# Kernel tuning notes

Measured on AMD Instinct MI355X. Metric: run time of the kernel, lower is better.

The kernel has to match this reference:

```python
import jax, jax.numpy as jnp
import numpy as np

B, N, D = 32, 2048, 512
Q, C = 8, 1024
COMMIT_W = 0.02


def setup_inputs() -> dict:
    key = jax.random.key(0)
    kx, kc = jax.random.split(key)
    x = jax.random.normal(kx, (B, N, D), dtype=jnp.float32)
    codebooks = jax.random.normal(kc, (Q, C, D), dtype=jnp.float32)  # per-quantizer embed tables
    return {"x": x, "codebooks": codebooks}


def _quantize(residual, embed):
    # residual: (B,N,D), embed: (C,D)
    flat = residual.reshape(-1, residual.shape[-1])  # (B*N, D)
    dist = (
        jnp.sum(flat * flat, axis=-1, keepdims=True)
        - 2.0 * (flat @ embed.T)
        + jnp.sum(embed * embed, axis=-1)
    )  # (B*N, C)
    idx = jnp.argmin(dist, axis=-1)  # (B*N,)
    q = embed[idx].reshape(residual.shape)  # codebook gather
    # commitment loss: mse(residual, stopgrad(quantized))
    commit = jnp.mean((jax.lax.stop_gradient(q) - residual) ** 2)
    # straight-through estimator
    q_st = residual + jax.lax.stop_gradient(q - residual)
    return idx.reshape(residual.shape[:-1]), q_st, commit


def reference(x, codebooks):
    residual = x
    quantized_out = jnp.zeros_like(x)
    all_indices = []
    all_losses = []
    for qi in range(Q):
        idx, quantized, commit = _quantize(residual, codebooks[qi])
        residual = residual - jax.lax.stop_gradient(quantized)
        quantized_out = quantized_out + quantized
        all_indices.append(idx)
        all_losses.append(commit * COMMIT_W)
    all_indices = jnp.stack(all_indices, axis=-1)  # (B, N, Q) int
    all_losses = jnp.stack(all_losses, axis=-1)  # (Q,)
    final_commit_loss = jnp.sum(all_losses)
    return quantized_out, all_indices, all_losses, final_commit_loss
```

## Files before the change

### kernel.cpp

```cpp
#include <hip/hip_runtime.h>

#define TOKENS   65536
#define DDIM     512
#define NQ       8
#define NCODES   1024
#define COMMIT_W 0.02

#define MT       32
#define NBLOCKS  (TOKENS / MT)
#define KSPLIT   384

#define OFF_IDX  ((size_t)TOKENS * DDIM)
#define OFF_LOSS (OFF_IDX + (size_t)TOKENS * NQ)
#define OFF_TOT  (OFF_LOSS + NQ)

typedef _Float16 f16;
typedef _Float16 f16x8 __attribute__((ext_vector_type(8)));
typedef float    f32x4 __attribute__((ext_vector_type(4)));

__device__ __forceinline__ bool better(float d, int i, float bd, int bi) {
  return (d < bd) || (d == bd && i < bi);
}

__device__ __forceinline__ void ins4(float dd, int c, float cd[4], int ci[4]) {
  if (better(dd, c, cd[3], ci[3])) {
    if (better(dd, c, cd[1], ci[1])) {
      if (better(dd, c, cd[0], ci[0])) {
        cd[3]=cd[2]; ci[3]=ci[2]; cd[2]=cd[1]; ci[2]=ci[1];
        cd[1]=cd[0]; ci[1]=ci[0]; cd[0]=dd; ci[0]=c;
      } else {
        cd[3]=cd[2]; ci[3]=ci[2]; cd[2]=cd[1]; ci[2]=ci[1];
        cd[1]=dd; ci[1]=c;
      }
    } else {
      if (better(dd, c, cd[2], ci[2])) { cd[3]=cd[2]; ci[3]=ci[2]; cd[2]=dd; ci[2]=c; }
      else { cd[3]=dd; ci[3]=c; }
    }
  }
}

__device__ __forceinline__ void merge4(float cd[4], int ci[4], const int m) {
  const float b0 = __shfl_xor(cd[0], m, 64), b1 = __shfl_xor(cd[1], m, 64),
              b2 = __shfl_xor(cd[2], m, 64), b3 = __shfl_xor(cd[3], m, 64);
  const int   o0 = __shfl_xor(ci[0], m, 64), o1 = __shfl_xor(ci[1], m, 64),
              o2 = __shfl_xor(ci[2], m, 64), o3 = __shfl_xor(ci[3], m, 64);
  float L0, L1, L2, L3; int M0, M1, M2, M3;
  if (better(b3, o3, cd[0], ci[0])) { L0 = b3; M0 = o3; } else { L0 = cd[0]; M0 = ci[0]; }
  if (better(b2, o2, cd[1], ci[1])) { L1 = b2; M1 = o2; } else { L1 = cd[1]; M1 = ci[1]; }
  if (better(b1, o1, cd[2], ci[2])) { L2 = b1; M2 = o1; } else { L2 = cd[2]; M2 = ci[2]; }
  if (better(b0, o0, cd[3], ci[3])) { L3 = b0; M3 = o0; } else { L3 = cd[3]; M3 = ci[3]; }
  if (better(L2, M2, L0, M0)) { float t=L0; L0=L2; L2=t; int u=M0; M0=M2; M2=u; }
  if (better(L3, M3, L1, M1)) { float t=L1; L1=L3; L3=t; int u=M1; M1=M3; M3=u; }
  if (better(L1, M1, L0, M0)) { float t=L0; L0=L1; L1=t; int u=M0; M0=M1; M1=u; }
  if (better(L3, M3, L2, M2)) { float t=L2; L2=L3; L3=t; int u=M2; M2=M3; M3=u; }
  cd[0]=L0; ci[0]=M0; cd[1]=L1; ci[1]=M1; cd[2]=L2; ci[2]=M2; cd[3]=L3; ci[3]=M3;
}

__device__ __forceinline__ float pw128_row_sq(const float* __restrict__ a) {
  float r0 = __fmul_rn(a[0], a[0]), r1 = __fmul_rn(a[1], a[1]);
  float r2 = __fmul_rn(a[2], a[2]), r3 = __fmul_rn(a[3], a[3]);
  float r4 = __fmul_rn(a[4], a[4]), r5 = __fmul_rn(a[5], a[5]);
  float r6 = __fmul_rn(a[6], a[6]), r7 = __fmul_rn(a[7], a[7]);
  for (int i = 8; i < 128; i += 8) {
    r0 = __fadd_rn(r0, __fmul_rn(a[i + 0], a[i + 0]));
    r1 = __fadd_rn(r1, __fmul_rn(a[i + 1], a[i + 1]));
    r2 = __fadd_rn(r2, __fmul_rn(a[i + 2], a[i + 2]));
    r3 = __fadd_rn(r3, __fmul_rn(a[i + 3], a[i + 3]));
    r4 = __fadd_rn(r4, __fmul_rn(a[i + 4], a[i + 4]));
    r5 = __fadd_rn(r5, __fmul_rn(a[i + 5], a[i + 5]));
    r6 = __fadd_rn(r6, __fmul_rn(a[i + 6], a[i + 6]));
    r7 = __fadd_rn(r7, __fmul_rn(a[i + 7], a[i + 7]));
  }
  return __fadd_rn(__fadd_rn(__fadd_rn(r0, r1), __fadd_rn(r2, r3)),
                   __fadd_rn(__fadd_rn(r4, r5), __fadd_rn(r6, r7)));
}

__global__ void prep_kernel(const float* __restrict__ cb, float* __restrict__ eef,
                            double* __restrict__ lossAcc) {
  const int code = blockIdx.x * blockDim.x + threadIdx.x;
  if (code == 0) {
#pragma unroll
    for (int j = 0; j < NQ; ++j) lossAcc[j] = 0.0;
  }
  if (code < NQ * NCODES) {
    const float* e = cb + (size_t)code * DDIM;
    const float p0 = pw128_row_sq(e), p1 = pw128_row_sq(e + 128);
    const float p2 = pw128_row_sq(e + 256), p3 = pw128_row_sq(e + 384);
    eef[code] = __fadd_rn(__fadd_rn(p0, p1), __fadd_rn(p2, p3));
  }
}

__global__ void cvt_kernel(const float* __restrict__ cb, f16* __restrict__ cbH) {
  const size_t base = ((size_t)blockIdx.x * 256 + threadIdx.x) * 8;
  const float4 v0 = *(const float4*)(cb + base);
  const float4 v1 = *(const float4*)(cb + base + 4);
  f16x8 h;
  h[0] = (f16)v0.x; h[1] = (f16)v0.y; h[2] = (f16)v0.z; h[3] = (f16)v0.w;
  h[4] = (f16)v1.x; h[5] = (f16)v1.y; h[6] = (f16)v1.z; h[7] = (f16)v1.w;
  *(f16x8*)(cbH + base) = h;
}

__global__ void __launch_bounds__(256, 2)
rvq_main(const float* __restrict__ x, const float* __restrict__ cb,
         const f16* __restrict__ cbH, const float* __restrict__ eef,
         double* __restrict__ lossAcc, float* __restrict__ outq,
         float* __restrict__ outidx) {
  __shared__ float  r_t[DDIM * MT];
  __shared__ __align__(16) char smem_u[MT * 128 * 2];
  __shared__ float  ee_lds[NCODES];
  __shared__ int    hist[MT][NQ];
  __shared__ double wred[4];

  f16*   ra  = (f16*)smem_u;
  float* wcd = (float*)smem_u;
  int*   wci = (int*)(smem_u + 2048);

  const int tid  = threadIdx.x;
  const int lane = tid & 63;
  const int wv   = tid >> 6;
  const int cbase = wv << 8;
  const int tokR = tid >> 3;
  const int part = tid & 7;
  const int blockTok = blockIdx.x * MT;

  {
    const int tm = tid & 31, kp = tid >> 5;
    const float* xr = x + (size_t)(blockTok + tm) * DDIM;
#pragma unroll
    for (int i = 0; i < 16; ++i) {
      const int d4 = (kp + i * 8) << 2;
      const float4 v = *(const float4*)(xr + d4);
      r_t[(d4 + 0) * MT + tm] = v.x;
      r_t[(d4 + 1) * MT + tm] = v.y;
      r_t[(d4 + 2) * MT + tm] = v.z;
      r_t[(d4 + 3) * MT + tm] = v.w;
    }
  }
  __syncthreads();

  const int la15 = lane & 15;
  const int kg8  = (lane >> 4) << 3;
  const int swz  = (la15 & 7) << 3;

  for (int qi = 0; qi < NQ; ++qi) {
    const float* cbq   = cb  + (size_t)qi * NCODES * DDIM;
    const f16*   cbq16 = cbH + (size_t)qi * NCODES * DDIM;
    const float* enq   = eef + qi * NCODES;

#pragma unroll
    for (int j = 0; j < 4; ++j) ee_lds[tid + j * 256] = enq[tid + j * 256];

    f32x4 acc[16][2];
#pragma unroll
    for (int mt = 0; mt < 16; ++mt) {
      acc[mt][0] = (f32x4){0.f, 0.f, 0.f, 0.f};
      acc[mt][1] = (f32x4){0.f, 0.f, 0.f, 0.f};
    }

    for (int ch = 0; ch < 4; ++ch) {
      __syncthreads();
      {
        const int tok  = tid & 31;
        const int ko   = tid >> 5;
        const int tswz = (tok & 7) << 3;
#pragma unroll
        for (int i = 0; i < 2; ++i) {
          const int kl = (ko + (i << 3)) << 3;
          const int kg = (ch << 7) + kl;
          f16x8 h;
#pragma unroll
          for (int j = 0; j < 8; ++j) h[j] = (f16)r_t[(kg + j) * MT + tok];
          *(f16x8*)&ra[tok * 128 + (kl ^ tswz)] = h;
        }
      }
      __syncthreads();
#pragma unroll
      for (int s = 0; s < 4; ++s) {
        const int kk = (s << 5) + kg8;
        const f16x8 b0 = *(const f16x8*)&ra[la15 * 128 + (kk ^ swz)];
        const f16x8 b1 = *(const f16x8*)&ra[(la15 + 16) * 128 + (kk ^ swz)];
        const f16* ap = cbq16 + (size_t)(cbase + la15) * DDIM + (ch << 7) + kk;
#pragma unroll
        for (int mt = 0; mt < 16; ++mt) {
          const f16x8 a = *(const f16x8*)(ap + (size_t)(mt << 4) * DDIM);
          acc[mt][0] = __builtin_amdgcn_mfma_f32_16x16x32_f16(a, b0, acc[mt][0], 0, 0, 0);
          acc[mt][1] = __builtin_amdgcn_mfma_f32_16x16x32_f16(a, b1, acc[mt][1], 0, 0, 0);
        }
      }
    }
    __syncthreads();

    float cd0[4], cd1[4]; int ci0[4], ci1[4];
#pragma unroll
    for (int s = 0; s < 4; ++s) {
      cd0[s] = 3.0e38f; ci0[s] = 0x7fffffff;
      cd1[s] = 3.0e38f; ci1[s] = 0x7fffffff;
    }
    const int rbase = cbase + ((lane >> 4) << 2);
#pragma unroll
    for (int mt = 0; mt < 16; ++mt) {
#pragma unroll
      for (int r = 0; r < 4; ++r) {
        const int code = rbase + (mt << 4) + r;
        const float eb = ee_lds[code];
        ins4(fmaf(-2.0f, acc[mt][0][r], eb), code, cd0, ci0);
        ins4(fmaf(-2.0f, acc[mt][1][r], eb), code, cd1, ci1);
      }
    }
    merge4(cd0, ci0, 16); merge4(cd0, ci0, 32);
    merge4(cd1, ci1, 16); merge4(cd1, ci1, 32);

    if (lane < 16) {
      const int w32 = wv << 5;
#pragma unroll
      for (int s = 0; s < 4; ++s) {
        wcd[(w32 + lane) * 4 + s]      = cd0[s];
        wci[(w32 + lane) * 4 + s]      = ci0[s];
        wcd[(w32 + lane + 16) * 4 + s] = cd1[s];
        wci[(w32 + lane + 16) * 4 + s] = ci1[s];
      }
    }
    __syncthreads();

    if (tid < 128) {
      const int tok4 = tid >> 2, cnd = tid & 3;
      float fd[4]; int fi[4];
#pragma unroll
      for (int s = 0; s < 4; ++s) { fd[s] = 3.0e38f; fi[s] = 0x7fffffff; }
      for (int w2 = 0; w2 < 4; ++w2) {
#pragma unroll
        for (int s = 0; s < 4; ++s) {
          const int e = ((w2 << 5) + tok4) * 4 + s;
          ins4(wcd[e], wci[e], fd, fi);
        }
      }
      const int cme = fi[cnd];

      float blk;
      {
        const int kb = cnd * 128;
        float a[8];
#pragma unroll
        for (int j = 0; j < 8; ++j) {
          const float v = r_t[(kb + j) * MT + tok4];
          a[j] = __fmul_rn(v, v);
        }
        for (int i = 8; i < 128; i += 8) {
#pragma unroll
          for (int j = 0; j < 8; ++j) {
            const float v = r_t[(kb + i + j) * MT + tok4];
            a[j] = __fadd_rn(a[j], __fmul_rn(v, v));
          }
        }
        blk = __fadd_rn(__fadd_rn(__fadd_rn(a[0], a[1]), __fadd_rn(a[2], a[3])),
                        __fadd_rn(__fadd_rn(a[4], a[5]), __fadd_rn(a[6], a[7])));
      }
      const float pw256 = __fadd_rn(blk, __shfl_xor(blk, 1, 64));
      const float rr    = __fadd_rn(pw256, __shfl_xor(pw256, 2, 64));

      const float* ep = cbq + (size_t)cme * DDIM;
      float Sa = 0.f, Sb = 0.f;
      for (int kb = 0; kb < DDIM; kb += 8) {
        const float4 e0 = *(const float4*)(ep + kb);
        const float4 e1 = *(const float4*)(ep + kb + 4);
        const float ev[8] = {e0.x, e0.y, e0.z, e0.w, e1.x, e1.y, e1.z, e1.w};
        float rv[8];
#pragma unroll
        for (int j = 0; j < 8; ++j) rv[j] = r_t[(kb + j) * MT + tok4];
        if (kb < KSPLIT) {
#pragma unroll
          for (int j = 0; j < 8; ++j) Sa = __fmaf_rn(rv[j], ev[j], Sa);
        } else {
#pragma unroll
          for (int j = 0; j < 8; ++j) Sb = __fmaf_rn(rv[j], ev[j], Sb);
        }
      }
      const float cross = __fadd_rn(Sa, Sb);
      const float u = __fsub_rn(rr, __fmul_rn(2.0f, cross));
      float dW = __fadd_rn(u, enq[cme]);
      int   cW = cme;
#pragma unroll
      for (int m = 1; m <= 2; m <<= 1) {
        const float od = __shfl_xor(dW, m, 64);
        const int   oc = __shfl_xor(cW, m, 64);
        if (better(od, oc, dW, cW)) { dW = od; cW = oc; }
      }
      if (cnd == 0) {
        hist[tok4][qi] = cW;
        outidx[(size_t)(blockTok + tok4) * NQ + qi] = (float)cW;
      }
    }
    __syncthreads();

    const int wc = hist[tokR][qi];
    const float* ew = cbq + (size_t)wc * DDIM;
    double lssq = 0.0;
    for (int i = 0; i < 16; ++i) {
      const int d4 = (part + i * 8) << 2;
      const float4 qv = *(const float4*)(ew + d4);
      const float qa[4] = {qv.x, qv.y, qv.z, qv.w};
#pragma unroll
      for (int e = 0; e < 4; ++e) {
        const float r  = r_t[(d4 + e) * MT + tokR];
        const float a  = __fsub_rn(qa[e], r);
        const float qs = __fadd_rn(r, a);
        const float rn = __fsub_rn(r, qs);
        r_t[(d4 + e) * MT + tokR] = rn;
        lssq += (double)a * (double)a;
      }
    }
#pragma unroll
    for (int off = 32; off; off >>= 1) lssq += __shfl_down(lssq, off, 64);
    if ((tid & 63) == 0) wred[tid >> 6] = lssq;
    __syncthreads();
    if (tid == 0) atomicAdd(&lossAcc[qi], wred[0] + wred[1] + wred[2] + wred[3]);
  }

  {
    for (int i = 0; i < 16; ++i) {
      const int d4 = (part + i * 8) << 2;
      const float4 xv = *(const float4*)(x + (size_t)(blockTok + tokR) * DDIM + d4);
      float r[4]  = {xv.x, xv.y, xv.z, xv.w};
      float qa[4] = {0.f, 0.f, 0.f, 0.f};
#pragma unroll
      for (int j = 0; j < NQ; ++j) {
        const int hj = hist[tokR][j];
        const float4 ev = *(const float4*)(cb + ((size_t)j * NCODES + hj) * DDIM + d4);
        const float qv[4] = {ev.x, ev.y, ev.z, ev.w};
#pragma unroll
        for (int e = 0; e < 4; ++e) {
          const float a  = __fsub_rn(qv[e], r[e]);
          const float qs = __fadd_rn(r[e], a);
          r[e]  = __fsub_rn(r[e], qs);
          qa[e] = __fadd_rn(qa[e], qs);
        }
      }
      float4 pk; pk.x = qa[0]; pk.y = qa[1]; pk.z = qa[2]; pk.w = qa[3];
      *(float4*)(outq + (size_t)(blockTok + tokR) * DDIM + d4) = pk;
    }
  }
}

__global__ void loss_fin(const double* __restrict__ lossAcc,
                         float* __restrict__ outLoss,
                         float* __restrict__ outTot) {
  if (threadIdx.x == 0 && blockIdx.x == 0) {
    double tot = 0.0;
    for (int qi = 0; qi < NQ; ++qi) {
      const double v = lossAcc[qi] * (COMMIT_W / ((double)TOKENS * (double)DDIM));
      outLoss[qi] = (float)v;
      tot += v;
    }
    *outTot = (float)tot;
  }
}

extern "C" void kernel_launch(void* const* d_in, const int* in_sizes, int n_in,
                              void* d_out, int out_size, void* d_ws, size_t ws_size,
                              hipStream_t stream) {
  const float* x  = (const float*)d_in[0];
  const float* cb = (const float*)d_in[1];
  float* out = (float*)d_out;

  double* lossAcc = (double*)d_ws;
  float*  eef     = (float*)((char*)d_ws + 256);
  f16*    cbH     = (f16*)((char*)d_ws + 65536);

  prep_kernel<<<dim3(32), dim3(256), 0, stream>>>(cb, eef, lossAcc);
  cvt_kernel<<<dim3(2048), dim3(256), 0, stream>>>(cb, cbH);
  rvq_main<<<dim3(NBLOCKS), dim3(256), 0, stream>>>(x, cb, cbH, eef, lossAcc,
                                                    out, out + OFF_IDX);
  loss_fin<<<dim3(1), dim3(64), 0, stream>>>(lossAcc, out + OFF_LOSS, out + OFF_TOT);
}
```

Before: 4.038 ms.

## Double block to 512 threads, halving per-wave codebook slice

```diff
diff --git a/kernel.cpp b/kernel.cpp
--- a/kernel.cpp
+++ b/kernel.cpp
@@ -7,6 +7,7 @@
 #define COMMIT_W 0.02
 
 #define MT       32
+#define NT       512
 #define NBLOCKS  (TOKENS / MT)
 #define KSPLIT   384
 
@@ -100,35 +101,33 @@
   *(f16x8*)(cbH + base) = h;
 }
 
-__global__ void __launch_bounds__(256, 2)
+__global__ void __launch_bounds__(NT, 4)
 rvq_main(const float* __restrict__ x, const float* __restrict__ cb,
          const f16* __restrict__ cbH, const float* __restrict__ eef,
          double* __restrict__ lossAcc, float* __restrict__ outq,
          float* __restrict__ outidx) {
   __shared__ float  r_t[DDIM * MT];
-  __shared__ __align__(16) char smem_u[MT * 128 * 2];
+  __shared__ __align__(16) char smem_u[8192];
   __shared__ float  ee_lds[NCODES];
   __shared__ int    hist[MT][NQ];
-  __shared__ double wred[4];
+  __shared__ double wred[8];
 
   f16*   ra  = (f16*)smem_u;
   float* wcd = (float*)smem_u;
-  int*   wci = (int*)(smem_u + 2048);
+  int*   wci = (int*)(smem_u + 4096);
 
   const int tid  = threadIdx.x;
   const int lane = tid & 63;
   const int wv   = tid >> 6;
-  const int cbase = wv << 8;
-  const int tokR = tid >> 3;
-  const int part = tid & 7;
+  const int cbase = wv << 7;
   const int blockTok = blockIdx.x * MT;
 
   {
     const int tm = tid & 31, kp = tid >> 5;
     const float* xr = x + (size_t)(blockTok + tm) * DDIM;
 #pragma unroll
-    for (int i = 0; i < 16; ++i) {
-      const int d4 = (kp + i * 8) << 2;
+    for (int i = 0; i < 8; ++i) {
+      const int d4 = (kp + i * 16) << 2;
       const float4 v = *(const float4*)(xr + d4);
       r_t[(d4 + 0) * MT + tm] = v.x;
       r_t[(d4 + 1) * MT + tm] = v.y;
@@ -148,11 +147,11 @@
     const float* enq   = eef + qi * NCODES;
 
 #pragma unroll
-    for (int j = 0; j < 4; ++j) ee_lds[tid + j * 256] = enq[tid + j * 256];
-
-    f32x4 acc[16][2];
-#pragma unroll
-    for (int mt = 0; mt < 16; ++mt) {
+    for (int j = 0; j < 2; ++j) ee_lds[tid + j * NT] = enq[tid + j * NT];
+
+    f32x4 acc[8][2];
+#pragma unroll
+    for (int mt = 0; mt < 8; ++mt) {
       acc[mt][0] = (f32x4){0.f, 0.f, 0.f, 0.f};
       acc[mt][1] = (f32x4){0.f, 0.f, 0.f, 0.f};
     }
@@ -163,15 +162,12 @@
         const int tok  = tid & 31;
         const int ko   = tid >> 5;
         const int tswz = (tok & 7) << 3;
-#pragma unroll
-        for (int i = 0; i < 2; ++i) {
-          const int kl = (ko + (i << 3)) << 3;
-          const int kg = (ch << 7) + kl;
-          f16x8 h;
-#pragma unroll
-          for (int j = 0; j < 8; ++j) h[j] = (f16)r_t[(kg + j) * MT + tok];
-          *(f16x8*)&ra[tok * 128 + (kl ^ tswz)] = h;
-        }
+        const int kl   = ko << 3;
+        const int kg   = (ch << 7) + kl;
+        f16x8 h;
+#pragma unroll
+        for (int j = 0; j < 8; ++j) h[j] = (f16)r_t[(kg + j) * MT + tok];
+        *(f16x8*)&ra[tok * 128 + (kl ^ tswz)] = h;
       }
       __syncthreads();
 #pragma unroll
@@ -181,7 +177,7 @@
         const f16x8 b1 = *(const f16x8*)&ra[(la15 + 16) * 128 + (kk ^ swz)];
         const f16* ap = cbq16 + (size_t)(cbase + la15) * DDIM + (ch << 7) + kk;
 #pragma unroll
-        for (int mt = 0; mt < 16; ++mt) {
+        for (int mt = 0; mt < 8; ++mt) {
           const f16x8 a = *(const f16x8*)(ap + (size_t)(mt << 4) * DDIM);
           acc[mt][0] = __builtin_amdgcn_mfma_f32_16x16x32_f16(a, b0, acc[mt][0], 0, 0, 0);
           acc[mt][1] = __builtin_amdgcn_mfma_f32_16x16x32_f16(a, b1, acc[mt][1], 0, 0, 0);
@@ -198,7 +194,7 @@
     }
     const int rbase = cbase + ((lane >> 4) << 2);
 #pragma unroll
-    for (int mt = 0; mt < 16; ++mt) {
+    for (int mt = 0; mt < 8; ++mt) {
 #pragma unroll
       for (int r = 0; r < 4; ++r) {
         const int code = rbase + (mt << 4) + r;
@@ -227,7 +223,7 @@
       float fd[4]; int fi[4];
 #pragma unroll
       for (int s = 0; s < 4; ++s) { fd[s] = 3.0e38f; fi[s] = 0x7fffffff; }
-      for (int w2 = 0; w2 < 4; ++w2) {
+      for (int w2 = 0; w2 < 8; ++w2) {
 #pragma unroll
         for (int s = 0; s < 4; ++s) {
           const int e = ((w2 << 5) + tok4) * 4 + s;
@@ -292,33 +288,46 @@
     }
     __syncthreads();
 
-    const int wc = hist[tokR][qi];
-    const float* ew = cbq + (size_t)wc * DDIM;
-    double lssq = 0.0;
-    for (int i = 0; i < 16; ++i) {
-      const int d4 = (part + i * 8) << 2;
-      const float4 qv = *(const float4*)(ew + d4);
-      const float qa[4] = {qv.x, qv.y, qv.z, qv.w};
-#pragma unroll
-      for (int e = 0; e < 4; ++e) {
-        const float r  = r_t[(d4 + e) * MT + tokR];
-        const float a  = __fsub_rn(qa[e], r);
-        const float qs = __fadd_rn(r, a);
-        const float rn = __fsub_rn(r, qs);
-        r_t[(d4 + e) * MT + tokR] = rn;
-        lssq += (double)a * (double)a;
-      }
-    }
-#pragma unroll
-    for (int off = 32; off; off >>= 1) lssq += __shfl_down(lssq, off, 64);
-    if ((tid & 63) == 0) wred[tid >> 6] = lssq;
+    {
+      const int utok = tid & 31;
+      const int ks   = tid >> 5;
+      const int wc = hist[utok][qi];
+      const float* ew = cbq + (size_t)wc * DDIM + (ks << 5);
+      double lssq = 0.0;
+#pragma unroll
+      for (int i = 0; i < 8; ++i) {
+        const float4 qv = *(const float4*)(ew + (i << 2));
+        const float qa[4] = {qv.x, qv.y, qv.z, qv.w};
+        const int k0 = (ks << 5) + (i << 2);
+#pragma unroll
+        for (int e = 0; e < 4; ++e) {
+          const float r  = r_t[(k0 + e) * MT + utok];
+          const float a  = __fsub_rn(qa[e], r);
+          const float qs = __fadd_rn(r, a);
+          const float rn = __fsub_rn(r, qs);
+          r_t[(k0 + e) * MT + utok] = rn;
+          lssq += (double)a * (double)a;
+        }
+      }
+#pragma unroll
+      for (int off = 32; off; off >>= 1) lssq += __shfl_down(lssq, off, 64);
+      if ((tid & 63) == 0) wred[tid >> 6] = lssq;
+    }
     __syncthreads();
-    if (tid == 0) atomicAdd(&lossAcc[qi], wred[0] + wred[1] + wred[2] + wred[3]);
+    if (tid == 0) {
+      double s = 0.0;
+#pragma unroll
+      for (int w = 0; w < 8; ++w) s += wred[w];
+      atomicAdd(&lossAcc[qi], s);
+    }
   }
 
   {
-    for (int i = 0; i < 16; ++i) {
-      const int d4 = (part + i * 8) << 2;
+    const int tokR = tid >> 4;
+    const int part = tid & 15;
+#pragma unroll
+    for (int i = 0; i < 8; ++i) {
+      const int d4 = (part + i * 16) << 2;
       const float4 xv = *(const float4*)(x + (size_t)(blockTok + tokR) * DDIM + d4);
       float r[4]  = {xv.x, xv.y, xv.z, xv.w};
       float qa[4] = {0.f, 0.f, 0.f, 0.f};
@@ -368,7 +377,7 @@
 
   prep_kernel<<<dim3(32), dim3(256), 0, stream>>>(cb, eef, lossAcc);
   cvt_kernel<<<dim3(2048), dim3(256), 0, stream>>>(cb, cbH);
-  rvq_main<<<dim3(NBLOCKS), dim3(256), 0, stream>>>(x, cb, cbH, eef, lossAcc,
-                                                    out, out + OFF_IDX);
+  rvq_main<<<dim3(NBLOCKS), dim3(NT), 0, stream>>>(x, cb, cbH, eef, lossAcc,
+                                                   out, out + OFF_IDX);
   loss_fin<<<dim3(1), dim3(64), 0, stream>>>(lossAcc, out + OFF_LOSS, out + OFF_TOT);
 }
```

Measured after the change: 3.462 ms. 14.3% less time.
